# Performance work log

Hardware: AMD Instinct MI355X
Metric: run time of the kernel (lower is better)

## Reference

```python
import jax, jax.numpy as jnp
import numpy as np

EPS = 1e-5

def _layernorm(x, gamma, beta):
    mu = jnp.mean(x, axis=-1, keepdims=True)
    var = jnp.var(x, axis=-1, keepdims=True)
    return (x - mu) * jax.lax.rsqrt(var + EPS) * gamma + beta

def setup_inputs() -> dict:
    key = jax.random.key(0)
    ks = jax.random.split(key, 6)
    B, S, N, c_m, c_z, H, c = 1, 512, 384, 64, 128, 8, 32
    return {
        "m_si": jax.random.normal(ks[0], (B, S, N, c_m), dtype=jnp.float32),
        "z_ij": jax.random.normal(ks[1], (B, N, N, c_z), dtype=jnp.float32),
        "gamma_m": jnp.ones((c_m,), dtype=jnp.float32),
        "beta_m": jnp.zeros((c_m,), dtype=jnp.float32),
        "W1": jax.random.normal(ks[2], (c_m, c * H), dtype=jnp.float32) * 0.05,
        "gamma_z": jnp.ones((c_z,), dtype=jnp.float32),
        "beta_z": jnp.zeros((c_z,), dtype=jnp.float32),
        "W2": jax.random.normal(ks[3], (c_z, H), dtype=jnp.float32) * 0.05,
        "W3": jax.random.normal(ks[4], (c_m, c * H), dtype=jnp.float32) * 0.05,
        "W4": jax.random.normal(ks[5], (c * H, c_m), dtype=jnp.float32) * 0.05,
    }

def reference(m_si, z_ij, gamma_m, beta_m, W1, gamma_z, beta_z, W2, W3, W4):
    B, S, N, c_m = m_si.shape
    H = W2.shape[-1]
    c = W1.shape[-1] // H
    m = _layernorm(m_si, gamma_m, beta_m)                 # [B,S,N,c_m]
    v = (m @ W1).reshape(B, S, N, H, c)                   # values  [B,S,N,H,c]
    g = jax.nn.sigmoid(m @ W3).reshape(B, S, N, H, c)     # gates   [B,S,N,H,c]
    b = _layernorm(z_ij, gamma_z, beta_z) @ W2            # pair bias [B,i,j,H]
    # original: softmax over dim=-2 of [B,H,i,j] i.e. over the i axis
    w = jax.nn.softmax(b, axis=1)                         # [B,i,j,H]
    # broadcast weighted average over tokens, shared across N_msa
    o = g * jnp.einsum('bijh,bsjhc->bsihc', w, v)         # [B,S,N,H,c]
    return o.reshape(B, S, N, H * c) @ W4                 # [B,S,N,c_m]
```

## Files before the change

### kernel.cpp

```cpp
#include <hip/hip_runtime.h>
#include <hip/hip_bf16.h>
#include <math.h>


typedef __attribute__((ext_vector_type(8))) short bf16x8;
typedef __attribute__((ext_vector_type(4))) float f32x4;
typedef unsigned int u32;

__device__ inline float b2f(short v) {
    union { float f; u32 u; } t; t.u = ((u32)(unsigned short)v) << 16; return t.f;
}

__global__ __launch_bounds__(256) void k0_prep(
    const float* __restrict__ W4, const float* __restrict__ W1,
    const float* __restrict__ W3,
    __hip_bfloat16* __restrict__ W4p,
    __hip_bfloat16* __restrict__ W13s)
{
    int idx = blockIdx.x * 256 + threadIdx.x;
    if (idx < 16384) {
        int d = idx >> 8, k = idx & 255;
        int koff = k & 31, h = k >> 5;
        int quad = koff >> 3, e = koff & 7;
        int c = (e < 4) ? (quad * 4 + e) : (16 + quad * 4 + (e - 4));
        int hc = h * 32 + c;
        W4p[idx] = __float2bfloat16(W4[hc * 64 + d]);
    } else {
        int t = idx - 16384;
        int n = t >> 6, k = t & 63;
        float v = (n < 256) ? W1[k * 256 + n] : W3[k * 256 + (n - 256)];
        int dst = n * 64 + ((((k >> 3) ^ (n & 7))) << 3) + (k & 7);
        W13s[dst] = __float2bfloat16(v);
    }
}

__global__ __launch_bounds__(256) void k1_ln_mv(
    const float* __restrict__ m_si,
    const float* __restrict__ gamma_m, const float* __restrict__ beta_m,
    const __hip_bfloat16* __restrict__ W13s,
    __hip_bfloat16* __restrict__ v_tg,
    __hip_bfloat16* __restrict__ g_p)
{
    __shared__ short a_t[128 * 64];
    __shared__ short b_t[512 * 64];
    const int bx = blockIdx.x;
    const int s = bx / 3, j0 = (bx % 3) * 128;
    const int tid = threadIdx.x;
    const int lane = tid & 63, wv = tid >> 6;
    const int col = lane & 15, quad = lane >> 4;

    {
        const short* src = (const short*)W13s;
        #pragma unroll
        for (int i = 0; i < 16; i++) {
            __builtin_amdgcn_global_load_lds(
                (const __attribute__((address_space(1))) u32*)
                    (src + i * 2048 + wv * 512 + lane * 8),
                (__attribute__((address_space(3))) u32*)(b_t + i * 2048 + wv * 512),
                16, 0, 0);
        }
    }

    {
        const float gm = gamma_m[lane], bm = beta_m[lane];
        const float* mrow = m_si + (size_t)(s * 384 + j0) * 64;
        const int cl = lane >> 3, e = lane & 7;
        #pragma unroll 4
        for (int rr = 0; rr < 32; rr++) {
            int r = wv * 32 + rr;
            float x = mrow[r * 64 + lane];
            float s1 = x, s2 = x * x;
            #pragma unroll
            for (int off = 32; off > 0; off >>= 1) {
                s1 += __shfl_xor(s1, off, 64);
                s2 += __shfl_xor(s2, off, 64);
            }
            float mu  = s1 * (1.0f / 64.0f);
            float var = s2 * (1.0f / 64.0f) - mu * mu;
            float rs  = rsqrtf(var + 1e-5f);
            __hip_bfloat16 mh = __float2bfloat16((x - mu) * rs * gm + bm);
            a_t[r * 64 + ((cl ^ (r & 7)) << 3) + e] = *(short*)&mh;
        }
    }
    __syncthreads();

    const int wm = wv >> 1, wn = wv & 1;

    bf16x8 mf[4][2];
    #pragma unroll
    for (int mt = 0; mt < 4; mt++) {
        int r = wm * 64 + mt * 16 + col;
        #pragma unroll
        for (int ks = 0; ks < 2; ks++) {
            int c = ks * 4 + quad;
            mf[mt][ks] = *(const bf16x8*)&a_t[r * 64 + ((c ^ (r & 7)) << 3)];
        }
    }

    short* vbase = (short*)v_tg + (size_t)s * 98304;
    __hip_bfloat16* gb = g_p + (size_t)s * 98304;

    #pragma unroll 1
    for (int step = 0; step < 4; step++) {
        bf16x8 wf[4][2];
        #pragma unroll
        for (int nt = 0; nt < 4; nt++) {
            int n = step * 128 + wn * 64 + nt * 16 + col;
            #pragma unroll
            for (int ks = 0; ks < 2; ks++) {
                int c = ks * 4 + quad;
                wf[nt][ks] = *(const bf16x8*)&b_t[n * 64 + ((c ^ (n & 7)) << 3)];
            }
        }

        if (step < 2) {
            f32x4 acc[4][4];
            #pragma unroll
            for (int nt = 0; nt < 4; nt++)
                #pragma unroll
                for (int mt = 0; mt < 4; mt++)
                    acc[nt][mt] = (f32x4){0.f, 0.f, 0.f, 0.f};
            #pragma unroll
            for (int ks = 0; ks < 2; ks++)
                #pragma unroll
                for (int nt = 0; nt < 4; nt++)
                    #pragma unroll
                    for (int mt = 0; mt < 4; mt++)
                        acc[nt][mt] = __builtin_amdgcn_mfma_f32_16x16x32_bf16(
                            wf[nt][ks], mf[mt][ks], acc[nt][mt], 0, 0, 0);
            #pragma unroll
            for (int nt = 0; nt < 4; nt++)
                #pragma unroll
                for (int mt = 0; mt < 4; mt++) {
                    int jg = j0 + wm * 64 + mt * 16 + col;
                    #pragma unroll
                    for (int reg = 0; reg < 4; reg++) {
                        int n = step * 128 + wn * 64 + nt * 16 + quad * 4 + reg;
                        __hip_bfloat16 t = __float2bfloat16(acc[nt][mt][reg]);
                        vbase[n * 384 + jg] = *(short*)&t;
                    }
                }
        } else {
            f32x4 acc[4][4];
            #pragma unroll
            for (int mt = 0; mt < 4; mt++)
                #pragma unroll
                for (int nt = 0; nt < 4; nt++)
                    acc[mt][nt] = (f32x4){0.f, 0.f, 0.f, 0.f};
            #pragma unroll
            for (int ks = 0; ks < 2; ks++)
                #pragma unroll
                for (int mt = 0; mt < 4; mt++)
                    #pragma unroll
                    for (int nt = 0; nt < 4; nt++)
                        acc[mt][nt] = __builtin_amdgcn_mfma_f32_16x16x32_bf16(
                            mf[mt][ks], wf[nt][ks], acc[mt][nt], 0, 0, 0);
            #pragma unroll
            for (int mt = 0; mt < 4; mt++)
                #pragma unroll
                for (int nt = 0; nt < 4; nt++) {
                    int n = (step - 2) * 128 + wn * 64 + nt * 16 + col;
                    int c32 = n & 31;
                    int koff = ((c32 & 15) >> 2) * 8 + (c32 & 3)
                             + ((c32 & 16) ? 4 : 0);
                    int kn = (n & ~31) | koff;
                    #pragma unroll
                    for (int reg = 0; reg < 4; reg++) {
                        int jg = j0 + wm * 64 + mt * 16 + quad * 4 + reg;
                        float gv = 1.0f / (1.0f + __expf(-acc[mt][nt][reg]));
                        gb[(size_t)jg * 256 + kn] = __float2bfloat16(gv);
                    }
                }
        }
    }
}

__global__ __launch_bounds__(256) void k2_ln_z(
    const float* __restrict__ z,
    const float* __restrict__ gamma_z, const float* __restrict__ beta_z,
    const float* __restrict__ W2, float* __restrict__ b_buf)
{
    const int tid = threadIdx.x;
    const int lane = tid & 63, wv = tid >> 6;
    const int R0 = blockIdx.x * 64;
    __shared__ float part[64][9];

    float2 g2 = *(const float2*)&gamma_z[lane * 2];
    float2 be2 = *(const float2*)&beta_z[lane * 2];
    float4 w2a = *(const float4*)&W2[lane * 16];
    float4 w2b = *(const float4*)&W2[lane * 16 + 4];
    float4 w2c = *(const float4*)&W2[lane * 16 + 8];
    float4 w2d = *(const float4*)&W2[lane * 16 + 12];

    const bool hi4 = (lane & 4) != 0;
    const bool hi2 = (lane & 2) != 0;
    const bool hi1 = (lane & 1) != 0;

    float2 zx = *(const float2*)&z[(size_t)(R0 + wv * 16) * 128 + lane * 2];
    #pragma unroll 1
    for (int rr = 0; rr < 16; rr++) {
        const int rl = wv * 16 + rr;
        float x0 = zx.x, x1 = zx.y;
        if (rr < 15)
            zx = *(const float2*)&z[(size_t)(R0 + rl + 1) * 128 + lane * 2];

        float s1 = x0 + x1, s2 = x0 * x0 + x1 * x1;
        #pragma unroll
        for (int off = 32; off > 0; off >>= 1) {
            s1 += __shfl_xor(s1, off, 64);
            s2 += __shfl_xor(s2, off, 64);
        }
        float mu  = s1 * (1.0f / 128.0f);
        float var = s2 * (1.0f / 128.0f) - mu * mu;
        float rs  = rsqrtf(var + 1e-5f);
        float mh0 = (x0 - mu) * rs * g2.x + be2.x;
        float mh1 = (x1 - mu) * rs * g2.y + be2.y;

        float p[8];
        p[0] = fmaf(mh0, w2a.x, mh1 * w2c.x);
        p[1] = fmaf(mh0, w2a.y, mh1 * w2c.y);
        p[2] = fmaf(mh0, w2a.z, mh1 * w2c.z);
        p[3] = fmaf(mh0, w2a.w, mh1 * w2c.w);
        p[4] = fmaf(mh0, w2b.x, mh1 * w2d.x);
        p[5] = fmaf(mh0, w2b.y, mh1 * w2d.y);
        p[6] = fmaf(mh0, w2b.z, mh1 * w2d.z);
        p[7] = fmaf(mh0, w2b.w, mh1 * w2d.w);

        float t[4];
        #pragma unroll
        for (int k = 0; k < 4; k++) {
            float keep = hi4 ? p[k + 4] : p[k];
            float send = hi4 ? p[k] : p[k + 4];
            t[k] = keep + __shfl_xor(send, 4, 64);
        }
        float u[2];
        #pragma unroll
        for (int k = 0; k < 2; k++) {
            float keep = hi2 ? t[k + 2] : t[k];
            float send = hi2 ? t[k] : t[k + 2];
            u[k] = keep + __shfl_xor(send, 2, 64);
        }
        float vsum;
        {
            float keep = hi1 ? u[1] : u[0];
            float send = hi1 ? u[0] : u[1];
            vsum = keep + __shfl_xor(send, 1, 64);
        }
        vsum += __shfl_xor(vsum, 8, 64);
        vsum += __shfl_xor(vsum, 16, 64);
        vsum += __shfl_xor(vsum, 32, 64);
        if (lane < 8) part[rl][lane] = vsum;
    }
    __syncthreads();

    {
        int h0 = tid >> 6, rl = tid & 63;
        b_buf[(size_t)h0 * 147456 + R0 + rl]       = part[rl][h0];
        b_buf[(size_t)(h0 + 4) * 147456 + R0 + rl] = part[rl][h0 + 4];
    }
}

__global__ __launch_bounds__(128) void k3a_part(
    const float* __restrict__ w_buf, float* __restrict__ pm, float* __restrict__ pl)
{
    const int h = blockIdx.x / 24, ic = blockIdx.x % 24;
    const int i0 = ic * 16;
    const int tid = threadIdx.x;
    const float* base = w_buf + ((size_t)h * 384 + i0) * 384;

    float m0 = -INFINITY, m1 = -INFINITY, m2 = -INFINITY;
    float l0 = 0.f, l1 = 0.f, l2 = 0.f;
    #pragma unroll 4
    for (int ii = 0; ii < 16; ii++) {
        float x0 = base[ii * 384 + tid];
        float x1 = base[ii * 384 + tid + 128];
        float x2 = base[ii * 384 + tid + 256];
        float n0 = fmaxf(m0, x0);
        l0 = l0 * __expf(m0 - n0) + __expf(x0 - n0); m0 = n0;
        float n1 = fmaxf(m1, x1);
        l1 = l1 * __expf(m1 - n1) + __expf(x1 - n1); m1 = n1;
        float n2 = fmaxf(m2, x2);
        l2 = l2 * __expf(m2 - n2) + __expf(x2 - n2); m2 = n2;
    }
    float* pmb = pm + ((size_t)h * 24 + ic) * 384;
    float* plb = pl + ((size_t)h * 24 + ic) * 384;
    pmb[tid]       = m0;  plb[tid]       = l0;
    pmb[tid + 128] = m1;  plb[tid + 128] = l1;
    pmb[tid + 256] = m2;  plb[tid + 256] = l2;
}

__global__ __launch_bounds__(384) void k3m_comb(
    const float* __restrict__ pm, const float* __restrict__ pl,
    float* __restrict__ Mf, float* __restrict__ invLf)
{
    const int h = blockIdx.x, j = threadIdx.x;
    float M = -INFINITY, L = 0.f;
    #pragma unroll 4
    for (int ic = 0; ic < 24; ic++) {
        float m = pm[((size_t)h * 24 + ic) * 384 + j];
        float l = pl[((size_t)h * 24 + ic) * 384 + j];
        float nM = fmaxf(M, m);
        L = L * __expf(M - nM) + l * __expf(m - nM);
        M = nM;
    }
    Mf[h * 384 + j] = M;
    invLf[h * 384 + j] = 1.0f / L;
}

__global__ __launch_bounds__(128) void k3b_write(
    const float* __restrict__ w_buf, const float* __restrict__ Mf,
    const float* __restrict__ invLf, __hip_bfloat16* __restrict__ w_bf)
{
    const int h = blockIdx.x / 24, ic = blockIdx.x % 24;
    const int i0 = ic * 16;
    const int tid = threadIdx.x;
    const float* base = w_buf + ((size_t)h * 384 + i0) * 384;
    __hip_bfloat16* ob = w_bf + ((size_t)h * 384 + i0) * 384;

    float M0 = Mf[h * 384 + tid],       iL0 = invLf[h * 384 + tid];
    float M1 = Mf[h * 384 + tid + 128], iL1 = invLf[h * 384 + tid + 128];
    float M2 = Mf[h * 384 + tid + 256], iL2 = invLf[h * 384 + tid + 256];
    #pragma unroll 4
    for (int ii = 0; ii < 16; ii++) {
        float x0 = base[ii * 384 + tid];
        float x1 = base[ii * 384 + tid + 128];
        float x2 = base[ii * 384 + tid + 256];
        ob[ii * 384 + tid]       = __float2bfloat16(__expf(x0 - M0) * iL0);
        ob[ii * 384 + tid + 128] = __float2bfloat16(__expf(x1 - M1) * iL1);
        ob[ii * 384 + tid + 256] = __float2bfloat16(__expf(x2 - M2) * iL2);
    }
}

__global__ __launch_bounds__(256, 3) void k4_mfma(
    const __hip_bfloat16* __restrict__ w_bf,
    const __hip_bfloat16* __restrict__ v_tg,
    const __hip_bfloat16* __restrict__ g_p,
    const __hip_bfloat16* __restrict__ W4p,
    float* __restrict__ out)
{
    __shared__ short v_t[2][12288];
    const int bx0 = blockIdx.x;
    const int bx = (bx0 & 7) * 384 + (bx0 >> 3);
    const int s = bx / 6, i0 = (bx % 6) * 64;
    const int tid = threadIdx.x;
    const int lane = tid & 63, wv = tid >> 6;
    const int col = lane & 15, quad = lane >> 4;
    const int swz = col & 7;

    int srow[6], skc[6];
    #pragma unroll
    for (int r = 0; r < 6; r++) {
        int p = r * 256 + tid;
        int row = p / 48;
        srow[r] = row;
        skc[r] = (p - row * 48) ^ (row & 7);
    }

    const short* vslab = (const short*)v_tg + (size_t)s * 98304;
    const short* wbase = (const short*)w_bf
        + (size_t)(i0 + wv * 16 + col) * 384 + quad * 8;

    auto STAGE = [&](int buf, int hh) {
        const short* src = vslab + hh * 12288;
        #pragma unroll
        for (int r = 0; r < 6; r++) {
            __builtin_amdgcn_global_load_lds(
                (const __attribute__((address_space(1))) u32*)
                    (src + srow[r] * 384 + skc[r] * 8),
                (__attribute__((address_space(3))) u32*)
                    (&v_t[buf][r * 2048 + wv * 512]),
                16, 0, 0);
        }
    };

    const short* gbase = (const short*)g_p
        + (size_t)(s * 384 + i0 + wv * 16 + col) * 256 + quad * 8;
    bf16x8 gf[8];
    #pragma unroll
    for (int h = 0; h < 8; h++)
        gf[h] = *(const bf16x8*)(gbase + h * 32);

    STAGE(0, 0);

    bf16x8 paf[8];

    #pragma unroll
    for (int h = 0; h < 8; h++) {
        __builtin_amdgcn_sched_barrier(0);
        asm volatile("s_waitcnt vmcnt(0)" ::: "memory");
        __builtin_amdgcn_s_barrier();
        __builtin_amdgcn_sched_barrier(0);

        bf16x8 wf[12];
        const short* wA = wbase + (size_t)h * 147456;
        #pragma unroll
        for (int ks = 0; ks < 12; ks++)
            wf[ks] = *(const bf16x8*)(wA + ks * 32);

        if (h < 7) STAGE((h + 1) & 1, h + 1);

        f32x4 a0v = {0.f, 0.f, 0.f, 0.f}, a1v = {0.f, 0.f, 0.f, 0.f};
        __builtin_amdgcn_s_setprio(1);
        #pragma unroll
        for (int ks = 0; ks < 12; ks++) {
            int ch = (ks * 4 + quad) ^ swz;
            bf16x8 a0 = *(const bf16x8*)&v_t[h & 1][col * 384 + ch * 8];
            bf16x8 a1 = *(const bf16x8*)&v_t[h & 1][(16 + col) * 384 + ch * 8];
            a0v = __builtin_amdgcn_mfma_f32_16x16x32_bf16(a0, wf[ks], a0v, 0, 0, 0);
            a1v = __builtin_amdgcn_mfma_f32_16x16x32_bf16(a1, wf[ks], a1v, 0, 0, 0);
        }
        __builtin_amdgcn_s_setprio(0);

        #pragma unroll
        for (int e = 0; e < 4; e++) {
            float v0 = a0v[e] * b2f(gf[h][e]);
            float v1 = a1v[e] * b2f(gf[h][4 + e]);
            __hip_bfloat16 t0 = __float2bfloat16(v0);
            __hip_bfloat16 t1 = __float2bfloat16(v1);
            paf[h][e]     = *(short*)&t0;
            paf[h][4 + e] = *(short*)&t1;
        }
    }

    f32x4 acc2[4];
    #pragma unroll
    for (int n = 0; n < 4; n++) acc2[n] = (f32x4){0.f, 0.f, 0.f, 0.f};
    #pragma unroll
    for (int h = 0; h < 8; h++) {
        #pragma unroll
        for (int n = 0; n < 4; n++) {
            bf16x8 b = *(const bf16x8*)((const short*)W4p
                        + (n * 16 + col) * 256 + h * 32 + quad * 8);
            acc2[n] = __builtin_amdgcn_mfma_f32_16x16x32_bf16(
                          paf[h], b, acc2[n], 0, 0, 0);
        }
    }
    float* obase = out + (size_t)(s * 384 + i0 + wv * 16 + quad * 4) * 64;
    #pragma unroll
    for (int n = 0; n < 4; n++)
        #pragma unroll
        for (int reg = 0; reg < 4; reg++)
            obase[reg * 64 + n * 16 + col] = acc2[n][reg];
}

extern "C" void kernel_launch(void* const* d_in, const int* in_sizes, int n_in,
                              void* d_out, int out_size, void* d_ws, size_t ws_size,
                              hipStream_t stream)
{
    const float* m_si    = (const float*)d_in[0];
    const float* z_ij    = (const float*)d_in[1];
    const float* gamma_m = (const float*)d_in[2];
    const float* beta_m  = (const float*)d_in[3];
    const float* W1      = (const float*)d_in[4];
    const float* gamma_z = (const float*)d_in[5];
    const float* beta_z  = (const float*)d_in[6];
    const float* W2      = (const float*)d_in[7];
    const float* W3      = (const float*)d_in[8];
    const float* W4      = (const float*)d_in[9];
    float* out = (float*)d_out;

    char* ws = (char*)d_ws;
    __hip_bfloat16* g_p  = (__hip_bfloat16*)ws;
    __hip_bfloat16* v_tg = (__hip_bfloat16*)(ws + 100663296);
    float*          w_buf = (float*)(ws + 201326592);
    __hip_bfloat16* W13s = (__hip_bfloat16*)(ws + 201326592);
    __hip_bfloat16* w_bf = (__hip_bfloat16*)(ws + 206045184);
    __hip_bfloat16* W4p  = (__hip_bfloat16*)(ws + 208404480);
    float* pm    = (float*)(ws + 208437248);
    float* pl    = (float*)(ws + 208732160);
    float* Mf    = (float*)(ws + 209027072);
    float* invLf = (float*)(ws + 209039360);

    k0_prep  <<<192,  256, 0, stream>>>(W4, W1, W3, W4p, W13s);
    k1_ln_mv <<<1536, 256, 0, stream>>>(m_si, gamma_m, beta_m, W13s, v_tg, g_p);
    k2_ln_z  <<<2304, 256, 0, stream>>>(z_ij, gamma_z, beta_z, W2, w_buf);
    k3a_part <<<192,  128, 0, stream>>>(w_buf, pm, pl);
    k3m_comb <<<8,    384, 0, stream>>>(pm, pl, Mf, invLf);
    k3b_write<<<192,  128, 0, stream>>>(w_buf, Mf, invLf, w_bf);
    k4_mfma  <<<3072, 256, 0, stream>>>(w_bf, v_tg, g_p, W4p, out);
}
```

Measured before the change: 516.3 us.

## Load v fragments directly from global memory instead of LDS double-buffering

Removes the LDS double-buffered staging of the v slab, along with its barriers and swizzle, in the k4 MFMA kernel. Each wave now reads its v fragments straight from global memory into registers, split into two halves so register pressure stays bounded. The gate fragments are also loaded per head instead of all up front. This drops the block-wide synchronization and LDS traffic, but all four waves now read the same v data separately from global/L2, and the load latency is no longer overlapped with compute.

```diff
diff --git a/kernel.cpp b/kernel.cpp
--- a/kernel.cpp
+++ b/kernel.cpp
@@ -338,85 +338,60 @@
     const __hip_bfloat16* __restrict__ W4p,
     float* __restrict__ out)
 {
-    __shared__ short v_t[2][12288];
     const int bx0 = blockIdx.x;
     const int bx = (bx0 & 7) * 384 + (bx0 >> 3);
     const int s = bx / 6, i0 = (bx % 6) * 64;
     const int tid = threadIdx.x;
     const int lane = tid & 63, wv = tid >> 6;
     const int col = lane & 15, quad = lane >> 4;
-    const int swz = col & 7;
-
-    int srow[6], skc[6];
-    #pragma unroll
-    for (int r = 0; r < 6; r++) {
-        int p = r * 256 + tid;
-        int row = p / 48;
-        srow[r] = row;
-        skc[r] = (p - row * 48) ^ (row & 7);
-    }
 
     const short* vslab = (const short*)v_tg + (size_t)s * 98304;
     const short* wbase = (const short*)w_bf
         + (size_t)(i0 + wv * 16 + col) * 384 + quad * 8;
-
-    auto STAGE = [&](int buf, int hh) {
-        const short* src = vslab + hh * 12288;
-        #pragma unroll
-        for (int r = 0; r < 6; r++) {
-            __builtin_amdgcn_global_load_lds(
-                (const __attribute__((address_space(1))) u32*)
-                    (src + srow[r] * 384 + skc[r] * 8),
-                (__attribute__((address_space(3))) u32*)
-                    (&v_t[buf][r * 2048 + wv * 512]),
-                16, 0, 0);
-        }
-    };
-
     const short* gbase = (const short*)g_p
         + (size_t)(s * 384 + i0 + wv * 16 + col) * 256 + quad * 8;
-    bf16x8 gf[8];
-    #pragma unroll
-    for (int h = 0; h < 8; h++)
-        gf[h] = *(const bf16x8*)(gbase + h * 32);
-
-    STAGE(0, 0);
+    const short* v0 = vslab + (     col) * 384 + quad * 8;
+    const short* v1 = vslab + (16 + col) * 384 + quad * 8;
 
     bf16x8 paf[8];
 
     #pragma unroll
     for (int h = 0; h < 8; h++) {
-        __builtin_amdgcn_sched_barrier(0);
-        asm volatile("s_waitcnt vmcnt(0)" ::: "memory");
-        __builtin_amdgcn_s_barrier();
-        __builtin_amdgcn_sched_barrier(0);
-
         bf16x8 wf[12];
         const short* wA = wbase + (size_t)h * 147456;
         #pragma unroll
         for (int ks = 0; ks < 12; ks++)
             wf[ks] = *(const bf16x8*)(wA + ks * 32);
-
-        if (h < 7) STAGE((h + 1) & 1, h + 1);
-
-        f32x4 a0v = {0.f, 0.f, 0.f, 0.f}, a1v = {0.f, 0.f, 0.f, 0.f};
+        bf16x8 gfh = *(const bf16x8*)(gbase + h * 32);
+
+        bf16x8 vf[12];
+        #pragma unroll
+        for (int ks = 0; ks < 12; ks++)
+            vf[ks] = *(const bf16x8*)(v0 + h * 12288 + ks * 32);
+        f32x4 a0v = {0.f, 0.f, 0.f, 0.f};
         __builtin_amdgcn_s_setprio(1);
         #pragma unroll
-        for (int ks = 0; ks < 12; ks++) {
-            int ch = (ks * 4 + quad) ^ swz;
-            bf16x8 a0 = *(const bf16x8*)&v_t[h & 1][col * 384 + ch * 8];
-            bf16x8 a1 = *(const bf16x8*)&v_t[h & 1][(16 + col) * 384 + ch * 8];
-            a0v = __builtin_amdgcn_mfma_f32_16x16x32_bf16(a0, wf[ks], a0v, 0, 0, 0);
-            a1v = __builtin_amdgcn_mfma_f32_16x16x32_bf16(a1, wf[ks], a1v, 0, 0, 0);
-        }
+        for (int ks = 0; ks < 12; ks++)
+            a0v = __builtin_amdgcn_mfma_f32_16x16x32_bf16(vf[ks], wf[ks], a0v, 0, 0, 0);
         __builtin_amdgcn_s_setprio(0);
 
+        bf16x8 uf[12];
+        #pragma unroll
+        for (int ks = 0; ks < 12; ks++)
+            uf[ks] = *(const bf16x8*)(v1 + h * 12288 + ks * 32);
+        f32x4 a1v = {0.f, 0.f, 0.f, 0.f};
+        __builtin_amdgcn_s_setprio(1);
+        #pragma unroll
+        for (int ks = 0; ks < 12; ks++)
+            a1v = __builtin_amdgcn_mfma_f32_16x16x32_bf16(uf[ks], wf[ks], a1v, 0, 0, 0);
+        __builtin_amdgcn_s_setprio(0);
+
         #pragma unroll
         for (int e = 0; e < 4; e++) {
-            float v0 = a0v[e] * b2f(gf[h][e]);
-            float v1 = a1v[e] * b2f(gf[h][4 + e]);
-            __hip_bfloat16 t0 = __float2bfloat16(v0);
-            __hip_bfloat16 t1 = __float2bfloat16(v1);
+            float v0f = a0v[e] * b2f(gfh[e]);
+            float v1f = a1v[e] * b2f(gfh[4 + e]);
+            __hip_bfloat16 t0 = __float2bfloat16(v0f);
+            __hip_bfloat16 t1 = __float2bfloat16(v1f);
             paf[h][e]     = *(short*)&t0;
             paf[h][4 + e] = *(short*)&t1;
         }
```

Measured after the change: 700.3 us. 35.6% more time.
